# Kernel tuning notes

Measured on AMD Instinct MI355X. Metric: run time of the kernel, lower is better.

Reference implementation:

```python
import jax, jax.numpy as jnp
import numpy as np

B, C, H, W = 8, 128, 64, 64


def _conv1x1(t, w, b):
    # t: [B,C,H,W], w: [O,C], b: [O]  (torch Conv2d k=1 weight squeezed)
    return jnp.einsum('bchw,oc->bohw', t, w) + b[None, :, None, None]


def setup_inputs() -> dict:
    key = jax.random.key(0)
    ks = jax.random.split(key, 6)
    s = 1.0 / np.sqrt(C)  # conv init scale
    return {
        'x': jax.random.normal(ks[0], (B, C, H, W), dtype=jnp.float32),
        'freq_weights': jnp.ones((C,), dtype=jnp.float32),
        'wq': jax.random.normal(ks[1], (C, C), dtype=jnp.float32) * s,
        'bq': jnp.zeros((C,), dtype=jnp.float32),
        'wk': jax.random.normal(ks[2], (C, C), dtype=jnp.float32) * s,
        'bk': jnp.zeros((C,), dtype=jnp.float32),
        'wv': jax.random.normal(ks[3], (C, C), dtype=jnp.float32) * s,
        'bv': jnp.zeros((C,), dtype=jnp.float32),
        'wo': jax.random.normal(ks[4], (C, C), dtype=jnp.float32) * s,
        'bo': jnp.zeros((C,), dtype=jnp.float32),
    }


def reference(x, freq_weights, wq, bq, wk, bk, wv, bv, wo, bo):
    b, c, h, w = x.shape
    n = h * w
    # FFT-domain magnitude reweighting (faithful abs/angle reconstruction)
    fd = jnp.fft.fft2(x, axes=(-2, -1))
    mag = jnp.abs(fd)
    freq_attn = mag * freq_weights[None, :, None, None]
    refined_freq = freq_attn * jnp.exp(1j * jnp.angle(fd))
    refined = jnp.fft.ifft2(refined_freq, axes=(-2, -1)).real.astype(x.dtype)
    # 1x1-conv Q/K/V projections
    q = _conv1x1(refined, wq, bq).reshape(b, c, n)
    k = _conv1x1(refined, wk, bk).reshape(b, c, n)
    v = _conv1x1(refined, wv, bv).reshape(b, c, n)
    # Spatial self-attention over HW tokens, features = channels
    scores = jnp.einsum('bcn,bcm->bnm', q, k) / jnp.sqrt(jnp.asarray(c, x.dtype))
    attn = jax.nn.softmax(scores, axis=-1)  # [B, HW, HW]
    out = jnp.einsum('bnm,bcm->bcn', attn, v).reshape(b, c, h, w)
    return _conv1x1(out, wo, bo)
```

## Files before the change

kernel.cpp:

```cpp
#include <hip/hip_runtime.h>
#include <hip/hip_bf16.h>
#include <math.h>


typedef __bf16 bf16;
typedef _Float16 f16;
typedef __bf16 bf16x8 __attribute__((ext_vector_type(8)));
typedef __bf16 bf16x4 __attribute__((ext_vector_type(4)));
typedef __bf16 bf16x2 __attribute__((ext_vector_type(2)));
typedef _Float16 f16x8 __attribute__((ext_vector_type(8)));
typedef float  f32x4  __attribute__((ext_vector_type(4)));
typedef unsigned int u32x4 __attribute__((ext_vector_type(4)));

#define MFMA16(a, b, c) __builtin_amdgcn_mfma_f32_16x16x32_bf16((a), (b), (c), 0, 0, 0)

static constexpr int BATCH = 8;
static constexpr int CH    = 128;
static constexpr int NTOK  = 4096;
static constexpr int XS    = 136;
static constexpr int VS    = 72;
static constexpr int PS2   = 40;
static constexpr int MS    = 136;
static constexpr float FIXM = 8.0f;

__device__ inline void dma16(const bf16* g, bf16* l) {
  __builtin_amdgcn_global_load_lds(
      (__attribute__((address_space(1))) unsigned int*)g,
      (__attribute__((address_space(3))) unsigned int*)l, 16, 0, 0);
}

__device__ inline bf16x8 cvt8(const float* p, float s) {
  f32x4 a = *(const f32x4*)p;
  f32x4 b = *(const f32x4*)(p + 4);
  bf16x8 r;
  #pragma unroll
  for (int i = 0; i < 4; ++i) { r[i] = (bf16)(a[i] * s); r[4 + i] = (bf16)(b[i] * s); }
  return r;
}

__global__ __launch_bounds__(512) void proj_kernel(
    const float* __restrict__ x, const float* __restrict__ fw,
    const float* __restrict__ wq, const float* __restrict__ wk,
    const float* __restrict__ wv,
    const float* __restrict__ bq, const float* __restrict__ bk,
    const float* __restrict__ bv,
    bf16* __restrict__ Qt, bf16* __restrict__ Kt, bf16* __restrict__ Vt,
    float qscale)
{
  const int wg = blockIdx.x;
  const int b = wg >> 6, tile = wg & 63;
  const int t = threadIdx.x;
  const int w = t >> 6, lane = t & 63, quad = lane >> 4, l15 = lane & 15;

  __shared__ bf16 stage[128 * VS];

  const float* xb = x + (size_t)b * CH * NTOK + tile * 64;
  #pragma unroll
  for (int i = 0; i < 8; ++i) {
    int c = (i * 8 + w) * 2;
    float f0 = fw[c], f1 = fw[c + 1];
    float x0 = xb[(size_t)c * NTOK + lane] * f0;
    float x1 = xb[(size_t)(c + 1) * NTOK + lane] * f1;
    bf16x2 pk; pk.x = (bf16)x0; pk.y = (bf16)x1;
    *(bf16x2*)(&stage[lane * XS + c]) = pk;
  }
  __syncthreads();

  bf16x8 xfrag[4][4];
  #pragma unroll
  for (int st = 0; st < 4; ++st)
    #pragma unroll
    for (int ks = 0; ks < 4; ++ks)
      xfrag[st][ks] = *(const bf16x8*)(&stage[(st * 16 + l15) * XS + ks * 32 + quad * 8]);

  const size_t wrow = (size_t)(w * 16 + l15) * CH;
  const int tokb = tile * 64;
  __syncthreads();

  {
    bf16x8 qw[4];
    #pragma unroll
    for (int ks = 0; ks < 4; ++ks) qw[ks] = cvt8(wq + wrow + ks * 32 + quad * 8, qscale);
    f32x4 acc[4];
    #pragma unroll
    for (int st = 0; st < 4; ++st) acc[st] = (f32x4){0.f, 0.f, 0.f, 0.f};
    #pragma unroll
    for (int ks = 0; ks < 4; ++ks)
      #pragma unroll
      for (int st = 0; st < 4; ++st)
        acc[st] = MFMA16(qw[ks], xfrag[st][ks], acc[st]);
    float bias[4];
    #pragma unroll
    for (int r = 0; r < 4; ++r) bias[r] = bq[w * 16 + quad * 4 + r] * qscale;
    #pragma unroll
    for (int st = 0; st < 4; ++st) {
      bf16x4 o;
      #pragma unroll
      for (int r = 0; r < 4; ++r) o[r] = (bf16)(acc[st][r] + bias[r]);
      *(bf16x4*)(&stage[(st * 16 + l15) * XS + w * 16 + quad * 4]) = o;
    }
    __syncthreads();
    #pragma unroll
    for (int p = 0; p < 2; ++p) {
      int idx = p * 512 + t, row = idx >> 4, ch = (idx & 15) * 8;
      u32x4 d = *(const u32x4*)(&stage[row * XS + ch]);
      *(u32x4*)(&Qt[((size_t)b * NTOK + tokb + row) * CH + ch]) = d;
    }
    __syncthreads();
  }
  {
    bf16x8 kw[4];
    #pragma unroll
    for (int ks = 0; ks < 4; ++ks) kw[ks] = cvt8(wk + wrow + ks * 32 + quad * 8, 1.0f);
    f32x4 acc[4];
    #pragma unroll
    for (int st = 0; st < 4; ++st) acc[st] = (f32x4){0.f, 0.f, 0.f, 0.f};
    #pragma unroll
    for (int ks = 0; ks < 4; ++ks)
      #pragma unroll
      for (int st = 0; st < 4; ++st)
        acc[st] = MFMA16(kw[ks], xfrag[st][ks], acc[st]);
    float bias[4];
    #pragma unroll
    for (int r = 0; r < 4; ++r) bias[r] = bk[w * 16 + quad * 4 + r];
    #pragma unroll
    for (int st = 0; st < 4; ++st) {
      bf16x4 o;
      #pragma unroll
      for (int r = 0; r < 4; ++r) o[r] = (bf16)(acc[st][r] + bias[r]);
      *(bf16x4*)(&stage[(st * 16 + l15) * XS + w * 16 + quad * 4]) = o;
    }
    __syncthreads();
    #pragma unroll
    for (int p = 0; p < 2; ++p) {
      int idx = p * 512 + t, row = idx >> 4, ch = (idx & 15) * 8;
      u32x4 d = *(const u32x4*)(&stage[row * XS + ch]);
      *(u32x4*)(&Kt[((size_t)b * NTOK + tokb + row) * CH + ch]) = d;
    }
    __syncthreads();
  }
  {
    bf16x8 vw[4];
    #pragma unroll
    for (int ks = 0; ks < 4; ++ks) vw[ks] = cvt8(wv + wrow + ks * 32 + quad * 8, 1.0f);
    f32x4 acc[4];
    #pragma unroll
    for (int st = 0; st < 4; ++st) acc[st] = (f32x4){0.f, 0.f, 0.f, 0.f};
    #pragma unroll
    for (int ks = 0; ks < 4; ++ks)
      #pragma unroll
      for (int st = 0; st < 4; ++st)
        acc[st] = MFMA16(xfrag[st][ks], vw[ks], acc[st]);
    float bias = bv[w * 16 + l15];
    #pragma unroll
    for (int st = 0; st < 4; ++st) {
      bf16x4 o;
      #pragma unroll
      for (int r = 0; r < 4; ++r) o[r] = (bf16)(acc[st][r] + bias);
      *(bf16x4*)(&stage[(w * 16 + l15) * VS + st * 16 + quad * 4]) = o;
    }
    __syncthreads();
    #pragma unroll
    for (int p = 0; p < 2; ++p) {
      int idx = p * 512 + t, row = idx >> 3, tk = (idx & 7) * 8;
      u32x4 d = *(const u32x4*)(&stage[row * VS + tk]);
      *(u32x4*)(&Vt[((size_t)b * CH + row) * NTOK + tokb + tk]) = d;
    }
  }
}

__global__ __launch_bounds__(256, 2) void flash_part_kernel(
    const bf16* __restrict__ Qt, const bf16* __restrict__ Kt,
    const bf16* __restrict__ Vt, f16* __restrict__ Op, float* __restrict__ Lp)
{
  __shared__ __align__(16) char lds[43008];

  const int wg = blockIdx.x;
  const int b = wg >> 6, half = (wg >> 5) & 1, qt = wg & 31;
  const int t = threadIdx.x;
  const int w = t >> 6, lane = t & 63, quad = lane >> 4, l15 = lane & 15;
  const int swz = l15 & 7;

  bf16x8 qfrag[2][4];
  #pragma unroll
  for (int s2 = 0; s2 < 2; ++s2) {
    const bf16* qb = Qt + ((size_t)b * NTOK + qt * 128 + w * 32 + s2 * 16 + l15) * CH;
    #pragma unroll
    for (int ks = 0; ks < 4; ++ks)
      qfrag[s2][ks] = *(const bf16x8*)(qb + ks * 32 + quad * 8);
  }

  f32x4 o_acc[2][8];
  #pragma unroll
  for (int s2 = 0; s2 < 2; ++s2)
    #pragma unroll
    for (int nt = 0; nt < 8; ++nt) o_acc[s2][nt] = (f32x4){0.f, 0.f, 0.f, 0.f};
  float lsum[2] = {0.f, 0.f};

  const bf16* kb = Kt + ((size_t)b * NTOK + half * 2048) * CH;
  const bf16* vb = Vt + (size_t)b * CH * NTOK + half * 2048;

  const bf16* kdma[2]; const bf16* vdma[2];
  #pragma unroll
  for (int jj = 0; jj < 2; ++jj) {
    int slot = w * 128 + jj * 64 + lane;
    int krow = slot >> 4, kcb = slot & 15;
    kdma[jj] = kb + (size_t)krow * CH + ((kcb ^ (krow & 7)) * 8);
    int vch = slot >> 2, vcb = slot & 3;
    vdma[jj] = vb + (size_t)vch * NTOK + (((vcb + ((vch >> 2) & 3)) & 3) * 8);
  }

  bf16* Pw = (bf16*)(lds + 32768) + w * 32 * PS2;

  {
    bf16* dK = (bf16*)(lds) + w * 1024;
    bf16* dV = (bf16*)(lds + 8192) + w * 1024;
    dma16(kdma[0], dK); dma16(kdma[1], dK + 512);
    dma16(vdma[0], dV); dma16(vdma[1], dV + 512);
    kdma[0] += 32 * CH; kdma[1] += 32 * CH;
    vdma[0] += 32;      vdma[1] += 32;
  }
  __syncthreads();

  for (int kt = 0; kt < 64; ++kt) {
    const char* bK = lds + ((kt & 1) ? 16384 : 0);
    const char* bV = bK + 8192;

    if (kt + 1 < 64) {
      bf16* nK = (bf16*)(lds + ((kt & 1) ? 0 : 16384)) + w * 1024;
      bf16* nV = nK + 4096;
      dma16(kdma[0], nK); dma16(kdma[1], nK + 512);
      dma16(vdma[0], nV); dma16(vdma[1], nV + 512);
      kdma[0] += 32 * CH; kdma[1] += 32 * CH;
      vdma[0] += 32;      vdma[1] += 32;
    }

    #pragma unroll
    for (int mt = 0; mt < 2; ++mt) {
      f32x4 s[2];
      s[0] = (f32x4){0.f, 0.f, 0.f, 0.f};
      s[1] = (f32x4){0.f, 0.f, 0.f, 0.f};
      #pragma unroll
      for (int ks = 0; ks < 4; ++ks) {
        bf16x8 kfr = *(const bf16x8*)(bK + (mt * 16 + l15) * 256 + (((ks * 4 + quad) ^ swz) * 16));
        s[0] = MFMA16(kfr, qfrag[0][ks], s[0]);
        s[1] = MFMA16(kfr, qfrag[1][ks], s[1]);
      }
      #pragma unroll
      for (int s2 = 0; s2 < 2; ++s2) {
        f32x4 v = s[s2];
        bf16x4 pk;
        float ps = 0.f;
        #pragma unroll
        for (int r = 0; r < 4; ++r) {
          float p = exp2f(v[r] - FIXM);
          ps += p;
          pk[r] = (bf16)p;
        }
        lsum[s2] += ps;
        *(bf16x4*)(Pw + (s2 * 16 + l15) * PS2 + mt * 16 + quad * 4) = pk;
      }
    }

    bf16x8 pfrag[2];
    #pragma unroll
    for (int s2 = 0; s2 < 2; ++s2)
      pfrag[s2] = *(const bf16x8*)(Pw + (s2 * 16 + l15) * PS2 + quad * 8);

    const int vrot = (l15 >> 2) & 3;
    const char* vrb = bV + l15 * 64 + (((quad - vrot) & 3) * 16);
    #pragma unroll
    for (int nt = 0; nt < 8; ++nt) {
      bf16x8 vfr = *(const bf16x8*)(vrb + nt * 1024);
      o_acc[0][nt] = MFMA16(pfrag[0], vfr, o_acc[0][nt]);
      o_acc[1][nt] = MFMA16(pfrag[1], vfr, o_acc[1][nt]);
    }

    __syncthreads();
  }

  const size_t obase = ((size_t)(b * 2 + half) * NTOK + qt * 128 + w * 32) * CH;
  #pragma unroll
  for (int s2 = 0; s2 < 2; ++s2)
    #pragma unroll
    for (int nt = 0; nt < 8; ++nt)
      #pragma unroll
      for (int r = 0; r < 4; ++r) {
        int row = s2 * 16 + quad * 4 + r;
        Op[obase + (size_t)row * CH + nt * 16 + l15] = (f16)o_acc[s2][nt][r];
      }
  #pragma unroll
  for (int s2 = 0; s2 < 2; ++s2) {
    float v = lsum[s2];
    v += __shfl_xor(v, 16);
    v += __shfl_xor(v, 32);
    if (quad == 0)
      Lp[(size_t)(b * 2 + half) * NTOK + qt * 128 + w * 32 + s2 * 16 + l15] = v;
  }
}

__global__ __launch_bounds__(256) void merge_kernel(
    const f16* __restrict__ Op, const float* __restrict__ Lp,
    const float* __restrict__ wo, const float* __restrict__ bo,
    float* __restrict__ out)
{
  const int wg = blockIdx.x;
  const int b = wg >> 6, tile = wg & 63;
  const int t = threadIdx.x;
  const int w = t >> 6, lane = t & 63, quad = lane >> 4, l15 = lane & 15;

  __shared__ bf16 ldsO[64 * MS];

  const f16* o0 = Op + ((size_t)(b * 2 + 0) * NTOK + tile * 64) * CH;
  const f16* o1 = Op + ((size_t)(b * 2 + 1) * NTOK + tile * 64) * CH;
  const float* lp0 = Lp + (size_t)(b * 2 + 0) * NTOK + tile * 64;
  const float* lp1 = Lp + (size_t)(b * 2 + 1) * NTOK + tile * 64;

  #pragma unroll
  for (int i = 0; i < 4; ++i) {
    int idx = t + i * 256;
    int row = idx >> 4, cb = idx & 15;
    float inv = 1.0f / (lp0[row] + lp1[row]);
    f16x8 a0 = *(const f16x8*)(o0 + (size_t)row * CH + cb * 8);
    f16x8 a1 = *(const f16x8*)(o1 + (size_t)row * CH + cb * 8);
    bf16 tmp[8];
    #pragma unroll
    for (int j = 0; j < 8; ++j)
      tmp[j] = (bf16)(((float)a0[j] + (float)a1[j]) * inv);
    *(u32x4*)(&ldsO[row * MS + cb * 8]) = *(u32x4*)tmp;
  }
  __syncthreads();

  #pragma unroll
  for (int mi = 0; mi < 2; ++mi) {
    int mt = w * 2 + mi;
    f32x4 facc[4];
    #pragma unroll
    for (int nt = 0; nt < 4; ++nt) facc[nt] = (f32x4){0.f, 0.f, 0.f, 0.f};
    #pragma unroll
    for (int ks = 0; ks < 4; ++ks) {
      bf16x8 afr = cvt8(wo + (size_t)(mt * 16 + l15) * CH + ks * 32 + quad * 8, 1.0f);
      #pragma unroll
      for (int nt = 0; nt < 4; ++nt) {
        bf16x8 bfr = *(const bf16x8*)(&ldsO[(nt * 16 + l15) * MS + ks * 32 + quad * 8]);
        facc[nt] = MFMA16(afr, bfr, facc[nt]);
      }
    }
    #pragma unroll
    for (int nt = 0; nt < 4; ++nt) {
      int n = tile * 64 + nt * 16 + l15;
      #pragma unroll
      for (int r = 0; r < 4; ++r) {
        int o = mt * 16 + quad * 4 + r;
        out[((size_t)b * CH + o) * NTOK + n] = facc[nt][r] + bo[o];
      }
    }
  }
}

extern "C" void kernel_launch(void* const* d_in, const int* in_sizes, int n_in,
                              void* d_out, int out_size, void* d_ws, size_t ws_size,
                              hipStream_t stream)
{
  const float* x  = (const float*)d_in[0];
  const float* fw = (const float*)d_in[1];
  const float* wq = (const float*)d_in[2];
  const float* bq = (const float*)d_in[3];
  const float* wk = (const float*)d_in[4];
  const float* bk = (const float*)d_in[5];
  const float* wv = (const float*)d_in[6];
  const float* bv = (const float*)d_in[7];
  const float* wo = (const float*)d_in[8];
  const float* bo = (const float*)d_in[9];
  float* out = (float*)d_out;

  char* ws = (char*)d_ws;
  bf16*  Qt  = (bf16*)ws;
  bf16*  Kt  = Qt + (size_t)BATCH * NTOK * CH;
  bf16*  Vt  = Kt + (size_t)BATCH * NTOK * CH;
  f16*   Op  = (f16*)(ws + 3ull * 8388608);
  float* Lp  = (float*)((char*)Op + 16777216);

  const float qscale = 0.08838834764831845f * 1.44269504f;

  proj_kernel<<<512, 512, 0, stream>>>(x, fw, wq, wk, wv,
                                       bq, bk, bv, Qt, Kt, Vt, qscale);
  flash_part_kernel<<<512, 256, 0, stream>>>(Qt, Kt, Vt, Op, Lp);
  merge_kernel<<<512, 256, 0, stream>>>(Op, Lp, wo, bo, out);
}
```

Measured before the change: 197.7 us.

## Generalize flash split-K to three key slabs with higher occupancy

The flash kernel no longer splits keys into exactly two halves. It now splits them into S slabs (three when the workspace is large enough, otherwise two), with an uneven tile split per slab. Launch bounds rise to three blocks per CU, and the grid grows to match, so more waves are resident to hide latency. The merge kernel now sums partial outputs and normalizers over all slabs. The cost is more fp16 partial-output traffic in the merge step, and a tighter register budget that could cause spills.

```diff
diff --git a/kernel.cpp b/kernel.cpp
--- a/kernel.cpp
+++ b/kernel.cpp
@@ -169,14 +169,19 @@
   }
 }
 
-__global__ __launch_bounds__(256, 2) void flash_part_kernel(
+__global__ __launch_bounds__(256, 3) void flash_part_kernel(
     const bf16* __restrict__ Qt, const bf16* __restrict__ Kt,
-    const bf16* __restrict__ Vt, f16* __restrict__ Op, float* __restrict__ Lp)
+    const bf16* __restrict__ Vt, f16* __restrict__ Op, float* __restrict__ Lp,
+    int nslab, int base, int rem)
 {
   __shared__ __align__(16) char lds[43008];
 
   const int wg = blockIdx.x;
-  const int b = wg >> 6, half = (wg >> 5) & 1, qt = wg & 31;
+  const int qt = wg & 31;
+  const int slab = (wg >> 5) % nslab;
+  const int b = wg / (nslab * 32);
+  const int ntile = base + (slab < rem ? 1 : 0);
+  const int koff  = (slab * base + (slab < rem ? slab : rem)) * 32;
   const int t = threadIdx.x;
   const int w = t >> 6, lane = t & 63, quad = lane >> 4, l15 = lane & 15;
   const int swz = l15 & 7;
@@ -197,8 +202,8 @@
     for (int nt = 0; nt < 8; ++nt) o_acc[s2][nt] = (f32x4){0.f, 0.f, 0.f, 0.f};
   float lsum[2] = {0.f, 0.f};
 
-  const bf16* kb = Kt + ((size_t)b * NTOK + half * 2048) * CH;
-  const bf16* vb = Vt + (size_t)b * CH * NTOK + half * 2048;
+  const bf16* kb = Kt + ((size_t)b * NTOK + koff) * CH;
+  const bf16* vb = Vt + (size_t)b * CH * NTOK + koff;
 
   const bf16* kdma[2]; const bf16* vdma[2];
   #pragma unroll
@@ -222,11 +227,11 @@
   }
   __syncthreads();
 
-  for (int kt = 0; kt < 64; ++kt) {
+  for (int kt = 0; kt < ntile; ++kt) {
     const char* bK = lds + ((kt & 1) ? 16384 : 0);
     const char* bV = bK + 8192;
 
-    if (kt + 1 < 64) {
+    if (kt + 1 < ntile) {
       bf16* nK = (bf16*)(lds + ((kt & 1) ? 0 : 16384)) + w * 1024;
       bf16* nV = nK + 4096;
       dma16(kdma[0], nK); dma16(kdma[1], nK + 512);
@@ -279,7 +284,7 @@
     __syncthreads();
   }
 
-  const size_t obase = ((size_t)(b * 2 + half) * NTOK + qt * 128 + w * 32) * CH;
+  const size_t obase = ((size_t)(slab * BATCH + b) * NTOK + qt * 128 + w * 32) * CH;
   #pragma unroll
   for (int s2 = 0; s2 < 2; ++s2)
     #pragma unroll
@@ -295,14 +300,14 @@
     v += __shfl_xor(v, 16);
     v += __shfl_xor(v, 32);
     if (quad == 0)
-      Lp[(size_t)(b * 2 + half) * NTOK + qt * 128 + w * 32 + s2 * 16 + l15] = v;
+      Lp[(size_t)(slab * BATCH + b) * NTOK + qt * 128 + w * 32 + s2 * 16 + l15] = v;
   }
 }
 
 __global__ __launch_bounds__(256) void merge_kernel(
     const f16* __restrict__ Op, const float* __restrict__ Lp,
     const float* __restrict__ wo, const float* __restrict__ bo,
-    float* __restrict__ out)
+    float* __restrict__ out, int nslab)
 {
   const int wg = blockIdx.x;
   const int b = wg >> 6, tile = wg & 63;
@@ -311,22 +316,27 @@
 
   __shared__ bf16 ldsO[64 * MS];
 
-  const f16* o0 = Op + ((size_t)(b * 2 + 0) * NTOK + tile * 64) * CH;
-  const f16* o1 = Op + ((size_t)(b * 2 + 1) * NTOK + tile * 64) * CH;
-  const float* lp0 = Lp + (size_t)(b * 2 + 0) * NTOK + tile * 64;
-  const float* lp1 = Lp + (size_t)(b * 2 + 1) * NTOK + tile * 64;
+  const size_t slabO = (size_t)BATCH * NTOK * CH;
+  const size_t slabL = (size_t)BATCH * NTOK;
+  const f16* ob = Op + ((size_t)b * NTOK + tile * 64) * CH;
+  const float* lp = Lp + (size_t)b * NTOK + tile * 64;
 
   #pragma unroll
   for (int i = 0; i < 4; ++i) {
     int idx = t + i * 256;
     int row = idx >> 4, cb = idx & 15;
-    float inv = 1.0f / (lp0[row] + lp1[row]);
-    f16x8 a0 = *(const f16x8*)(o0 + (size_t)row * CH + cb * 8);
-    f16x8 a1 = *(const f16x8*)(o1 + (size_t)row * CH + cb * 8);
+    float lsum_ = 0.f;
+    for (int s = 0; s < nslab; ++s) lsum_ += lp[s * slabL + row];
+    float acc8[8] = {0.f, 0.f, 0.f, 0.f, 0.f, 0.f, 0.f, 0.f};
+    for (int s = 0; s < nslab; ++s) {
+      f16x8 a = *(const f16x8*)(ob + s * slabO + (size_t)row * CH + cb * 8);
+      #pragma unroll
+      for (int j = 0; j < 8; ++j) acc8[j] += (float)a[j];
+    }
+    float inv = 1.0f / lsum_;
     bf16 tmp[8];
     #pragma unroll
-    for (int j = 0; j < 8; ++j)
-      tmp[j] = (bf16)(((float)a0[j] + (float)a1[j]) * inv);
+    for (int j = 0; j < 8; ++j) tmp[j] = (bf16)(acc8[j] * inv);
     *(u32x4*)(&ldsO[row * MS + cb * 8]) = *(u32x4*)tmp;
   }
   __syncthreads();
@@ -379,12 +389,19 @@
   bf16*  Kt  = Qt + (size_t)BATCH * NTOK * CH;
   bf16*  Vt  = Kt + (size_t)BATCH * NTOK * CH;
   f16*   Op  = (f16*)(ws + 3ull * 8388608);
-  float* Lp  = (float*)((char*)Op + 16777216);
+
+  const size_t qkv_bytes = 3ull * 8388608;
+  const size_t need3 = qkv_bytes + 3ull * ((size_t)BATCH * NTOK * CH * 2 + (size_t)BATCH * NTOK * 4);
+  const int S = (ws_size >= need3) ? 3 : 2;
+  const int base = 128 / S, rem = 128 % S;
+
+  float* Lp = (float*)((char*)Op + (size_t)S * BATCH * NTOK * CH * 2);
 
   const float qscale = 0.08838834764831845f * 1.44269504f;
 
   proj_kernel<<<512, 512, 0, stream>>>(x, fw, wq, wk, wv,
                                        bq, bk, bv, Qt, Kt, Vt, qscale);
-  flash_part_kernel<<<512, 256, 0, stream>>>(Qt, Kt, Vt, Op, Lp);
-  merge_kernel<<<512, 256, 0, stream>>>(Op, Lp, wo, bo, out);
-}
+  flash_part_kernel<<<BATCH * S * 32, 256, 0, stream>>>(Qt, Kt, Vt, Op, Lp,
+                                                        S, base, rem);
+  merge_kernel<<<512, 256, 0, stream>>>(Op, Lp, wo, bo, out, S);
+}
```

After: 194.6 us. No clear change (-1.6%).
